# Kernel tuning notes

Measured on AMD Instinct MI355X. Metric: run time of the kernel, lower is better.

Reference implementation:

```python
import jax, jax.numpy as jnp
import numpy as np

BETA_MEM = 0.9
BETA_INH = 0.6
THRESHOLD = 1.0  # snn.Leaky default


def setup_inputs() -> dict:
    key = jax.random.key(0)
    k1, = jax.random.split(key, 1)
    T, B = 1024, 16384
    spike_seq = (jax.random.uniform(k1, (T, B, 2)) < 0.05).astype(jnp.float32)
    w_exc = jnp.array([[0.7, 1.0]], dtype=jnp.float32)  # fc_exc.weight, [1, 2]
    w_inh = jnp.array(-1.0, dtype=jnp.float32)          # scalar inhibitory weight
    return {"spike_seq": spike_seq, "w_exc": w_exc, "w_inh": w_inh}


@jax.custom_vjp
def spike_fn(x):
    # Heaviside spike with ATan surrogate gradient (snntorch default, alpha=2)
    return (x > 0).astype(x.dtype)

def _spike_fwd(x):
    return spike_fn(x), x

def _spike_bwd(x, g):
    return (g / (1.0 + (jnp.pi * x) ** 2),)

spike_fn.defvjp(_spike_fwd, _spike_bwd)


def reference(spike_seq, w_exc, w_inh):
    T, B, _ = spike_seq.shape
    mem0 = jnp.zeros((B, 1), dtype=spike_seq.dtype)
    inh0 = jnp.zeros((B, 1), dtype=spike_seq.dtype)

    def step(carry, x_t):
        mem, inh = carry
        cur_exc = x_t @ w_exc.T                      # [B, 1]
        fm1 = x_t[:, 0:1]                            # [B, 1]
        inh = BETA_INH * inh + fm1
        cur = cur_exc + w_inh * inh
        # snn.Leaky: reset (subtract) computed from previous mem, detached
        reset = jax.lax.stop_gradient((mem - THRESHOLD > 0).astype(mem.dtype))
        mem = BETA_MEM * mem + cur - reset * THRESHOLD
        spk = spike_fn(mem - THRESHOLD)
        return (mem, inh), (spk, mem)

    _, (spk_rec, mem_rec) = jax.lax.scan(step, (mem0, inh0), spike_seq)
    return spk_rec, mem_rec  # each [T, B, 1]
```

## Files before the change

### kernel.cpp

```cpp
#include <hip/hip_runtime.h>

#define T_LEN 1024
#define B_N   16384
#define PH    16
#define NPH   (T_LEN / PH)

__shared__ __align__(16) float2 OUT_lds[4][PH][64];

static __device__ __forceinline__ void block_barrier() {
  asm volatile("" ::: "memory");
  __builtin_amdgcn_s_barrier();
  asm volatile("" ::: "memory");
}

__global__ __launch_bounds__(256, 1) void FMFMNeuronInhib_34033320854098_kernel(
    const float* __restrict__ x,
    const float* __restrict__ w_exc,
    const float* __restrict__ w_inh,
    float* __restrict__ out) {
#pragma clang fp contract(off)
  const int lane = threadIdx.x & 63;
  const int wid  = threadIdx.x >> 6;
  const int nb0  = blockIdx.x * 64;

  float* __restrict__ spk_out = out;
  float* __restrict__ mem_out = out + (size_t)T_LEN * B_N;

  if (wid == 0) {
    const float w0 = w_exc[0];
    const float w1 = w_exc[1];
    const float wi = w_inh[0];
    const float2* __restrict__ xp = (const float2*)x + nb0 + lane;
    float mem = 0.0f, inh = 0.0f;

    float2 bufA[PH], bufB[PH];
#pragma unroll
    for (int u = 0; u < PH; ++u) bufA[u] = xp[(size_t)u * B_N];
#pragma unroll
    for (int u = 0; u < PH; ++u) bufB[u] = xp[(size_t)(PH + u) * B_N];
    __builtin_amdgcn_sched_barrier(0);

    auto phase = [&](float2 (&buf)[PH], int p) {
#pragma clang fp contract(off)
#pragma unroll
      for (int u = 0; u < PH; ++u) {
        const float x0 = buf[u].x;
        const float x1 = buf[u].y;
        const float cur_exc = x0 * w0 + x1 * w1;
        inh = 0.6f * inh + x0;
        const float cur = cur_exc + wi * inh;
        const float reset = (mem > 1.0f) ? 1.0f : 0.0f;
        mem = 0.9f * mem + cur - reset;
        const float spk = (mem > 1.0f) ? 1.0f : 0.0f;
        OUT_lds[p & 3][u][lane] = make_float2(spk, mem);
      }
      __builtin_amdgcn_sched_barrier(0);
      if (p + 2 < NPH) {
#pragma unroll
        for (int u = 0; u < PH; ++u)
          buf[u] = xp[(size_t)((p + 2) * PH + u) * B_N];
      }
      __builtin_amdgcn_sched_barrier(0);
      asm volatile("s_waitcnt lgkmcnt(0)" ::: "memory");
      block_barrier();
    };

    for (int p = 0; p < NPH; p += 2) {
      phase(bufA, p);
      phase(bufB, p + 1);
    }
  } else {
    const int sid = wid - 1;
    auto drain = [&](int p) {
      const int tb = p * PH;
      const int slot = p & 3;
#pragma unroll
      for (int u = 0; u < PH; ++u) {
        const float2 v = OUT_lds[slot][u][lane];
        const size_t idx = (size_t)(tb + u) * B_N + nb0 + lane;
        spk_out[idx] = v.x;
        mem_out[idx] = v.y;
      }
    };
    for (int p = 0; p < NPH; ++p) {
      if (p >= 1 && ((p - 1) % 3) == sid) drain(p - 1);
      block_barrier();
    }
    if ((NPH - 1) % 3 == sid) drain(NPH - 1);
  }
}

extern "C" void kernel_launch(void* const* d_in, const int* in_sizes, int n_in,
                              void* d_out, int out_size, void* d_ws, size_t ws_size,
                              hipStream_t stream) {
  const float* x     = (const float*)d_in[0];
  const float* w_exc = (const float*)d_in[1];
  const float* w_inh = (const float*)d_in[2];
  float* out = (float*)d_out;

  dim3 grid(B_N / 64);
  dim3 block(256);
  hipLaunchKernelGGL(FMFMNeuronInhib_34033320854098_kernel, grid, block, 0, stream,
                     x, w_exc, w_inh, out);
}
```

Before: 246.8 us.

## Replace block barriers with LDS flag-based producer/consumer pipeline and async global-to-LDS loads

Adds a dedicated loader wavefront that streams input into a 5-slot LDS ring using global_load_lds. The compute wave and two drain waves now synchronise through workgroup-scope acquire/release flags instead of a full block barrier per phase. The aim is to decouple the serial recurrence wave from load latency and store throughput, so it no longer stalls on the slowest wave each phase. In exchange it adds spin-wait polling with s_sleep and more complex ring-slot bookkeeping, and drops from three drain waves to two.

```diff
diff --git a/kernel.cpp b/kernel.cpp
--- a/kernel.cpp
+++ b/kernel.cpp
@@ -4,13 +4,20 @@
 #define B_N   16384
 #define PH    16
 #define NPH   (T_LEN / PH)
+#define RIN   5
+#define ROUT  2
+#define WGSC  __HIP_MEMORY_SCOPE_WORKGROUP
 
-__shared__ __align__(16) float2 OUT_lds[4][PH][64];
 
-static __device__ __forceinline__ void block_barrier() {
-  asm volatile("" ::: "memory");
-  __builtin_amdgcn_s_barrier();
-  asm volatile("" ::: "memory");
+__shared__ __align__(16) float2 IN_lds[RIN][PH][64];
+__shared__ __align__(16) float2 OUT_lds[ROUT][PH][64];
+__shared__ int F[8];
+
+static __device__ __forceinline__ int ld_flag(int i) {
+  return __hip_atomic_load(&F[i], __ATOMIC_ACQUIRE, WGSC);
+}
+static __device__ __forceinline__ void st_flag(int i, int v) {
+  __hip_atomic_store(&F[i], v, __ATOMIC_RELEASE, WGSC);
 }
 
 __global__ __launch_bounds__(256, 1) void FMFMNeuronInhib_34033320854098_kernel(
@@ -23,70 +30,83 @@
   const int wid  = threadIdx.x >> 6;
   const int nb0  = blockIdx.x * 64;
 
+  if (threadIdx.x < 8) F[threadIdx.x] = 0;
+  __syncthreads();
+
   float* __restrict__ spk_out = out;
   float* __restrict__ mem_out = out + (size_t)T_LEN * B_N;
 
-  if (wid == 0) {
+  if (wid == 1) {
+    const int half = lane >> 5;
+    const int l32  = lane & 31;
+    for (int p = 0; p < NPH; ++p) {
+      while (ld_flag(1) < p - (RIN - 1)) __builtin_amdgcn_s_sleep(1);
+      const int slot = p % RIN;
+#pragma unroll
+      for (int j = 0; j < 8; ++j) {
+        const int t = p * PH + 2 * j + half;
+        const float* src = x + ((size_t)t * B_N + nb0) * 2 + (size_t)l32 * 4;
+        __builtin_amdgcn_global_load_lds(
+            (const __attribute__((address_space(1))) void*)src,
+            (__attribute__((address_space(3))) void*)&IN_lds[slot][2 * j][0],
+            16, 0, 0);
+      }
+      if (p >= 4) {
+        asm volatile("s_waitcnt vmcnt(32)" ::: "memory");
+        if (lane == 0) st_flag(0, p - 3);
+      }
+    }
+    asm volatile("s_waitcnt vmcnt(0)" ::: "memory");
+    if (lane == 0) st_flag(0, NPH);
+  } else if (wid == 0) {
     const float w0 = w_exc[0];
     const float w1 = w_exc[1];
     const float wi = w_inh[0];
-    const float2* __restrict__ xp = (const float2*)x + nb0 + lane;
     float mem = 0.0f, inh = 0.0f;
+    for (int p = 0; p < NPH; ++p) {
+      while (ld_flag(0) < p + 1) __builtin_amdgcn_s_sleep(1);
+      const int islot = p % RIN;
+      float2 xv[PH];
+#pragma unroll
+      for (int u = 0; u < PH; ++u) xv[u] = IN_lds[islot][u][lane];
+      if (lane == 0) st_flag(1, p + 1);
 
-    float2 bufA[PH], bufB[PH];
-#pragma unroll
-    for (int u = 0; u < PH; ++u) bufA[u] = xp[(size_t)u * B_N];
-#pragma unroll
-    for (int u = 0; u < PH; ++u) bufB[u] = xp[(size_t)(PH + u) * B_N];
-    __builtin_amdgcn_sched_barrier(0);
-
-    auto phase = [&](float2 (&buf)[PH], int p) {
-#pragma clang fp contract(off)
+      float sv[PH], mv[PH];
 #pragma unroll
       for (int u = 0; u < PH; ++u) {
-        const float x0 = buf[u].x;
-        const float x1 = buf[u].y;
+        const float x0 = xv[u].x;
+        const float x1 = xv[u].y;
         const float cur_exc = x0 * w0 + x1 * w1;
         inh = 0.6f * inh + x0;
         const float cur = cur_exc + wi * inh;
         const float reset = (mem > 1.0f) ? 1.0f : 0.0f;
         mem = 0.9f * mem + cur - reset;
-        const float spk = (mem > 1.0f) ? 1.0f : 0.0f;
-        OUT_lds[p & 3][u][lane] = make_float2(spk, mem);
+        sv[u] = (mem > 1.0f) ? 1.0f : 0.0f;
+        mv[u] = mem;
       }
-      __builtin_amdgcn_sched_barrier(0);
-      if (p + 2 < NPH) {
+      if (p >= ROUT)
+        while (ld_flag(3 + (p & 1)) < p - 1) __builtin_amdgcn_s_sleep(1);
+      const int oslot = p % ROUT;
 #pragma unroll
-        for (int u = 0; u < PH; ++u)
-          buf[u] = xp[(size_t)((p + 2) * PH + u) * B_N];
-      }
-      __builtin_amdgcn_sched_barrier(0);
-      asm volatile("s_waitcnt lgkmcnt(0)" ::: "memory");
-      block_barrier();
-    };
-
-    for (int p = 0; p < NPH; p += 2) {
-      phase(bufA, p);
-      phase(bufB, p + 1);
+      for (int u = 0; u < PH; ++u)
+        OUT_lds[oslot][u][lane] = make_float2(sv[u], mv[u]);
+      if (lane == 0) st_flag(2, p + 1);
     }
   } else {
-    const int sid = wid - 1;
-    auto drain = [&](int p) {
+    const int sid = wid - 2;
+    for (int p = sid; p < NPH; p += 2) {
+      while (ld_flag(2) < p + 1) __builtin_amdgcn_s_sleep(1);
+      const int oslot = p & 1;
       const int tb = p * PH;
-      const int slot = p & 3;
 #pragma unroll
       for (int u = 0; u < PH; ++u) {
-        const float2 v = OUT_lds[slot][u][lane];
+        const float2 v = OUT_lds[oslot][u][lane];
         const size_t idx = (size_t)(tb + u) * B_N + nb0 + lane;
         spk_out[idx] = v.x;
         mem_out[idx] = v.y;
       }
-    };
-    for (int p = 0; p < NPH; ++p) {
-      if (p >= 1 && ((p - 1) % 3) == sid) drain(p - 1);
-      block_barrier();
+      if (lane == 0) st_flag(3 + sid, p + 1);
     }
-    if ((NPH - 1) % 3 == sid) drain(NPH - 1);
   }
 }
 
```

Measured after the change: 243.5 us. Within noise of the previous version (-1.3%).

## Bit-pack spikes, checkpoint states, and parallelize scan over time segments

Applied to the files above, without the earlier changes.

Splits the work into three kernels. The first packs the binary input spikes into bitmasks. The second runs the recurrence over the packed bits and saves (mem, inh) checkpoints at segment boundaries. The third recomputes eight time segments in parallel from those checkpoints and writes the outputs through LDS using float4 stores. The goal is to expose more parallelism than the original 256-block serial scan and to cut input bandwidth, at the cost of two extra launches, a workspace buffer, and a serial checkpoint pass that still covers most of the time steps.

```diff
diff --git a/kernel.cpp b/kernel.cpp
--- a/kernel.cpp
+++ b/kernel.cpp
@@ -2,10 +2,74 @@
 
 #define T_LEN 1024
 #define B_N   16384
-#define PH    16
-#define NPH   (T_LEN / PH)
+#define NSEG  8
+#define SEGT  (T_LEN / NSEG)
+#define GN    256
+#define PH2   8
+#define NPH2  (SEGT / PH2)
+#define CW_WORDS (B_N * (T_LEN / 16))
 
-__shared__ __align__(16) float2 OUT_lds[4][PH][64];
+__global__ __launch_bounds__(256) void k1_compress(
+    const float* __restrict__ x, unsigned int* __restrict__ cw) {
+  const int tid = blockIdx.x * 256 + threadIdx.x;
+  const int pn  = tid & (B_N / 2 - 1);
+  const int j   = tid >> 13;
+  const float4* xp4 = (const float4*)x;
+  unsigned int wA = 0, wB = 0;
+#pragma unroll
+  for (int k = 0; k < 16; ++k) {
+    const float4 v = xp4[(size_t)(16 * j + k) * (B_N / 2) + pn];
+    wA |= (v.x != 0.0f ? 1u : 0u) << (2 * k);
+    wA |= (v.y != 0.0f ? 1u : 0u) << (2 * k + 1);
+    wB |= (v.z != 0.0f ? 1u : 0u) << (2 * k);
+    wB |= (v.w != 0.0f ? 1u : 0u) << (2 * k + 1);
+  }
+  ((uint2*)cw)[(size_t)j * (B_N / 2) + pn] = make_uint2(wA, wB);
+}
+
+__global__ __launch_bounds__(64, 1) void k2a_checkpoint(
+    const unsigned int* __restrict__ cw,
+    const float* __restrict__ w_exc, const float* __restrict__ w_inh,
+    float2* __restrict__ chk) {
+#pragma clang fp contract(off)
+  const int n = blockIdx.x * 64 + threadIdx.x;
+  const float w0 = w_exc[0], w1 = w_exc[1], wi = w_inh[0];
+  float mem = 0.0f, inh = 0.0f;
+  unsigned int A = cw[n];
+  unsigned int Bw = cw[(size_t)1 * B_N + n];
+  unsigned int C = cw[(size_t)2 * B_N + n];
+  unsigned int D = cw[(size_t)3 * B_N + n];
+
+#define STEP16(W)                                                   \
+  _Pragma("unroll") for (int k = 0; k < 16; ++k) {                  \
+    const float x0 = (float)(((W) >> (2 * k)) & 1u);                \
+    const float x1 = (float)(((W) >> (2 * k + 1)) & 1u);            \
+    const float cur_exc = x0 * w0 + x1 * w1;   \
+    inh = 0.6f * inh + x0;                                          \
+    const float cur = cur_exc + wi * inh;          \
+    const float reset = (mem > 1.0f) ? 1.0f : 0.0f;                 \
+    mem = 0.9f * mem + cur - reset;           \
+  }
+
+  for (int j = 0; j < 56; j += 4) {
+    unsigned int nA = 0, nB = 0, nC = 0, nD = 0;
+    if (j + 4 < 56) {
+      nA = cw[(size_t)(j + 4) * B_N + n];
+      nB = cw[(size_t)(j + 5) * B_N + n];
+      nC = cw[(size_t)(j + 6) * B_N + n];
+      nD = cw[(size_t)(j + 7) * B_N + n];
+    }
+    __builtin_amdgcn_sched_barrier(0);
+    STEP16(A) STEP16(Bw) STEP16(C) STEP16(D)
+    if (((j + 4) & 7) == 0)
+      chk[(size_t)(((j + 4) >> 3) - 1) * B_N + n] = make_float2(mem, inh);
+    A = nA; Bw = nB; C = nC; D = nD;
+  }
+#undef STEP16
+}
+
+__shared__ __align__(16) float SPK[2][PH2][GN];
+__shared__ __align__(16) float MEM[2][PH2][GN];
 
 static __device__ __forceinline__ void block_barrier() {
   asm volatile("" ::: "memory");
@@ -13,80 +77,72 @@
   asm volatile("" ::: "memory");
 }
 
-__global__ __launch_bounds__(256, 1) void FMFMNeuronInhib_34033320854098_kernel(
-    const float* __restrict__ x,
-    const float* __restrict__ w_exc,
-    const float* __restrict__ w_inh,
+__global__ __launch_bounds__(384, 1) void FMFMNeuronInhib_34033320854098_kernel(
+    const unsigned int* __restrict__ cw, const float2* __restrict__ chk,
+    const float* __restrict__ w_exc, const float* __restrict__ w_inh,
     float* __restrict__ out) {
 #pragma clang fp contract(off)
   const int lane = threadIdx.x & 63;
   const int wid  = threadIdx.x >> 6;
-  const int nb0  = blockIdx.x * 64;
+  const int seg  = blockIdx.x >> 6;
+  const int g    = blockIdx.x & 63;
+  const int nb0  = g * GN;
+  const int tseg = seg * SEGT;
 
-  float* __restrict__ spk_out = out;
-  float* __restrict__ mem_out = out + (size_t)T_LEN * B_N;
-
-  if (wid == 0) {
-    const float w0 = w_exc[0];
-    const float w1 = w_exc[1];
-    const float wi = w_inh[0];
-    const float2* __restrict__ xp = (const float2*)x + nb0 + lane;
+  if (wid < 4) {
+    const int nloc = wid * 64 + lane;
+    const int n    = nb0 + nloc;
+    const float w0 = w_exc[0], w1 = w_exc[1], wi = w_inh[0];
     float mem = 0.0f, inh = 0.0f;
-
-    float2 bufA[PH], bufB[PH];
+    if (seg > 0) {
+      const float2 c = chk[(size_t)(seg - 1) * B_N + n];
+      mem = c.x; inh = c.y;
+    }
+    unsigned int wcur = cw[(size_t)(seg * 8) * B_N + n];
+    for (int jl = 0; jl < 8; ++jl) {
+      unsigned int wnext = 0u;
+      if (jl < 7) wnext = cw[(size_t)(seg * 8 + jl + 1) * B_N + n];
 #pragma unroll
-    for (int u = 0; u < PH; ++u) bufA[u] = xp[(size_t)u * B_N];
+      for (int half = 0; half < 2; ++half) {
 #pragma unroll
-    for (int u = 0; u < PH; ++u) bufB[u] = xp[(size_t)(PH + u) * B_N];
-    __builtin_amdgcn_sched_barrier(0);
-
-    auto phase = [&](float2 (&buf)[PH], int p) {
-#pragma clang fp contract(off)
-#pragma unroll
-      for (int u = 0; u < PH; ++u) {
-        const float x0 = buf[u].x;
-        const float x1 = buf[u].y;
-        const float cur_exc = x0 * w0 + x1 * w1;
-        inh = 0.6f * inh + x0;
-        const float cur = cur_exc + wi * inh;
-        const float reset = (mem > 1.0f) ? 1.0f : 0.0f;
-        mem = 0.9f * mem + cur - reset;
-        const float spk = (mem > 1.0f) ? 1.0f : 0.0f;
-        OUT_lds[p & 3][u][lane] = make_float2(spk, mem);
+        for (int u = 0; u < 8; ++u) {
+          const int k = half * 8 + u;
+          const float x0 = (float)((wcur >> (2 * k)) & 1u);
+          const float x1 = (float)((wcur >> (2 * k + 1)) & 1u);
+          const float cur_exc = x0 * w0 + x1 * w1;
+          inh = 0.6f * inh + x0;
+          const float cur = cur_exc + wi * inh;
+          const float reset = (mem > 1.0f) ? 1.0f : 0.0f;
+          mem = 0.9f * mem + cur - reset;
+          const float spk = (mem > 1.0f) ? 1.0f : 0.0f;
+          SPK[half][u][nloc] = spk;
+          MEM[half][u][nloc] = mem;
+        }
+        asm volatile("s_waitcnt lgkmcnt(0)" ::: "memory");
+        block_barrier();
       }
-      __builtin_amdgcn_sched_barrier(0);
-      if (p + 2 < NPH) {
-#pragma unroll
-        for (int u = 0; u < PH; ++u)
-          buf[u] = xp[(size_t)((p + 2) * PH + u) * B_N];
-      }
-      __builtin_amdgcn_sched_barrier(0);
-      asm volatile("s_waitcnt lgkmcnt(0)" ::: "memory");
-      block_barrier();
-    };
-
-    for (int p = 0; p < NPH; p += 2) {
-      phase(bufA, p);
-      phase(bufB, p + 1);
+      wcur = wnext;
     }
   } else {
-    const int sid = wid - 1;
+    float* gout = (wid == 4) ? out : out + (size_t)T_LEN * B_N;
+    const float* plane = (wid == 4) ? &SPK[0][0][0] : &MEM[0][0][0];
+    const int n0 = lane * 4;
     auto drain = [&](int p) {
-      const int tb = p * PH;
-      const int slot = p & 3;
+      const int slot = p & 1;
+      const int t0   = tseg + p * PH2;
 #pragma unroll
-      for (int u = 0; u < PH; ++u) {
-        const float2 v = OUT_lds[slot][u][lane];
-        const size_t idx = (size_t)(tb + u) * B_N + nb0 + lane;
-        spk_out[idx] = v.x;
-        mem_out[idx] = v.y;
+      for (int r = 0; r < PH2; ++r) {
+        const float4 v =
+            *(const float4*)(plane + ((size_t)slot * PH2 + r) * GN + n0);
+        *(float4*)&gout[(size_t)(t0 + r) * B_N + nb0 + n0] = v;
       }
+      asm volatile("s_waitcnt lgkmcnt(0)" ::: "memory");
     };
-    for (int p = 0; p < NPH; ++p) {
-      if (p >= 1 && ((p - 1) % 3) == sid) drain(p - 1);
+    for (int p = 0; p < NPH2; ++p) {
+      if (p >= 1) drain(p - 1);
       block_barrier();
     }
-    if ((NPH - 1) % 3 == sid) drain(NPH - 1);
+    drain(NPH2 - 1);
   }
 }
 
@@ -97,9 +153,14 @@
   const float* w_exc = (const float*)d_in[1];
   const float* w_inh = (const float*)d_in[2];
   float* out = (float*)d_out;
+  unsigned int* cw = (unsigned int*)d_ws;
+  float2* chk = (float2*)((char*)d_ws + (size_t)CW_WORDS * 4);
 
-  dim3 grid(B_N / 64);
-  dim3 block(256);
-  hipLaunchKernelGGL(FMFMNeuronInhib_34033320854098_kernel, grid, block, 0, stream,
-                     x, w_exc, w_inh, out);
+  hipLaunchKernelGGL(k1_compress, dim3(CW_WORDS / 2 / 256), dim3(256), 0,
+                     stream, x, cw);
+  hipLaunchKernelGGL(k2a_checkpoint, dim3(B_N / 64), dim3(64), 0, stream,
+                     cw, w_exc, w_inh, chk);
+  hipLaunchKernelGGL(FMFMNeuronInhib_34033320854098_kernel,
+                     dim3(NSEG * (B_N / GN)), dim3(384), 0, stream,
+                     cw, chk, w_exc, w_inh, out);
 }
```

Measured after the change: 270.9 us. 9.8% more time.
